# Kernel tuning notes

Measured on AMD Instinct MI355X. Metric: run time of the kernel, lower is better.

## Reference

```python
import jax, jax.numpy as jnp
import numpy as np

B, S, H, D = 2, 2048, 16, 64


def setup_inputs() -> dict:
    key = jax.random.key(0)
    ks = jax.random.split(key, 6)
    query = jax.random.normal(ks[0], (B, S, H, D), dtype=jnp.float32)
    k = jax.random.normal(ks[1], (B, S, H, D), dtype=jnp.float32)
    v = jax.random.normal(ks[2], (B, S, H, D), dtype=jnp.float32)
    r = jax.random.normal(ks[3], (B, S, H, D), dtype=jnp.float32)
    r_bias = jax.random.normal(ks[4], (H, D), dtype=jnp.float32)
    r_w_bias = jax.random.normal(ks[5], (H, D), dtype=jnp.float32)
    # causal mask, broadcast over batch and heads; mask==0 positions are filled with -1e9
    mask = jnp.tril(jnp.ones((S, S), dtype=jnp.int32))[None, None, :, :]
    return {"query": query, "key": k, "value": v, "r": r,
            "r_bias": r_bias, "r_w_bias": r_w_bias, "mask": mask}


def reference(query, key, value, r, r_bias, r_w_bias, mask):
    b, s, h, d = query.shape
    # content-based and position-based query terms (Transformer-XL u/v biases)
    rw_head_q = jnp.transpose(query + r_w_bias, (0, 2, 1, 3))  # [B,H,S,D]
    rr_head_q = jnp.transpose(query + r_bias, (0, 2, 1, 3))    # [B,H,S,D]
    k_t = jnp.transpose(key, (0, 2, 1, 3))                     # [B,H,S,D]
    r_t = jnp.transpose(r.reshape(b, -1, h, d), (0, 2, 1, 3))  # [B,H,R,D]
    AC = jnp.einsum('bhqd,bhkd->bhqk', rw_head_q, k_t)
    BD = jnp.einsum('bhqd,bhkd->bhqk', rr_head_q, r_t)
    scores = (AC + BD) * (1.0 / np.sqrt(d).astype(np.float32))
    scores = jnp.where(mask == 0, jnp.float32(-1e9), scores)
    p_attn = jax.nn.softmax(scores, axis=-1)
    v_t = jnp.transpose(value, (0, 2, 1, 3))                   # [B,H,S,D]
    out = jnp.einsum('bhqk,bhkd->bhqd', p_attn, v_t)
    return out, p_attn
```

## Files before the change

kernel.cpp:

```cpp
#include <hip/hip_runtime.h>
#include <hip/hip_fp16.h>

#define S_LEN 2048
#define DHEAD 64
#define NBH   32
#define NHEADS 16

typedef _Float16 half_t;
typedef half_t half8  __attribute__((ext_vector_type(8)));
typedef half_t half4v __attribute__((ext_vector_type(4)));
typedef __fp16 fp16x2 __attribute__((ext_vector_type(2)));
typedef float  f32x16 __attribute__((ext_vector_type(16)));
typedef float  f32x4  __attribute__((ext_vector_type(4)));

#define QSCALE 0.18033688011112042f

__global__ __launch_bounds__(256) void prep_kernel(
    const float* __restrict__ q, const float* __restrict__ k,
    const float* __restrict__ v, const float* __restrict__ r,
    const float* __restrict__ r_bias, const float* __restrict__ r_w_bias,
    half_t* __restrict__ qh, half_t* __restrict__ krh,
    half_t* __restrict__ vt, float* __restrict__ c2)
{
    __shared__ float vtile[64][65];
    int blk = blockIdx.x;
    int st  = blk & 31;
    int bh  = blk >> 5;
    int b = bh >> 4, h = bh & 15;
    int s0 = st * 64;
    int t = threadIdx.x;
    int dg = t & 15;
    int rw = t >> 4;
    const float4 ub = *(const float4*)(r_w_bias + h * 64 + 4 * dg);
    const float4 vb = *(const float4*)(r_bias   + h * 64 + 4 * dg);
    #pragma unroll
    for (int ps = 0; ps < 4; ++ps) {
        int row = ps * 16 + rw;
        size_t iidx = ((size_t)((b * S_LEN + s0 + row) * NHEADS + h)) * DHEAD + 4 * dg;
        float4 qv = *(const float4*)(q + iidx);
        float4 kv = *(const float4*)(k + iidx);
        float4 rv = *(const float4*)(r + iidx);
        float4 vv = *(const float4*)(v + iidx);
        size_t oidx = ((size_t)(bh * S_LEN + s0 + row)) * DHEAD + 4 * dg;
        half4v hq  = { (half_t)(qv.x * QSCALE), (half_t)(qv.y * QSCALE),
                       (half_t)(qv.z * QSCALE), (half_t)(qv.w * QSCALE) };
        half4v hkr = { (half_t)(kv.x + rv.x), (half_t)(kv.y + rv.y),
                       (half_t)(kv.z + rv.z), (half_t)(kv.w + rv.w) };
        *(half4v*)(qh  + oidx) = hq;
        *(half4v*)(krh + oidx) = hkr;
        vtile[4 * dg + 0][row] = vv.x;
        vtile[4 * dg + 1][row] = vv.y;
        vtile[4 * dg + 2][row] = vv.z;
        vtile[4 * dg + 3][row] = vv.w;
        float part = ub.x * kv.x + ub.y * kv.y + ub.z * kv.z + ub.w * kv.w
                   + vb.x * rv.x + vb.y * rv.y + vb.z * rv.z + vb.w * rv.w;
        #pragma unroll
        for (int mm = 1; mm <= 8; mm <<= 1) part += __shfl_xor(part, mm, 64);
        if (dg == 0) c2[(size_t)bh * S_LEN + s0 + row] = part * QSCALE;
    }
    __syncthreads();
    {
        int d = t >> 2, j0 = (t & 3) * 16;
        const float* src = &vtile[d][j0];
        half8 h0, h1;
        #pragma unroll
        for (int e = 0; e < 8; ++e) { h0[e] = (half_t)src[e]; h1[e] = (half_t)src[8 + e]; }
        half_t* dst = vt + ((size_t)(bh * DHEAD + d)) * S_LEN + s0 + j0;
        *(half8*)(dst)     = h0;
        *(half8*)(dst + 8) = h1;
    }
}

__global__ __launch_bounds__(256) void attn_kernel(
    const half_t* __restrict__ qh, const half_t* __restrict__ krh,
    const half_t* __restrict__ vt, const float* __restrict__ c2,
    float* __restrict__ dout)
{
    __shared__ float zl[4][64];
    __shared__ f32x4 pvred[2][8][64];

    int bb  = blockIdx.x;
    int bh  = (bb & 7) * 4 + ((bb >> 3) & 3);
    int qt  = 63 - (bb >> 5);
    int i0  = qt * 32;
    int w    = threadIdx.x >> 6;
    int lane = threadIdx.x & 63;
    int lo = lane & 31, hi = lane >> 5;
    int qrow = i0 + lo;

    const half_t* qp = qh  + ((size_t)(bh * S_LEN + i0)) * DHEAD;
    const half_t* kp = krh + ((size_t)bh * S_LEN) * DHEAD;
    const half_t* vp = vt  + ((size_t)bh * DHEAD) * S_LEN;
    const float*  cp = c2  + (size_t)bh * S_LEN;
    float* pout = dout + (size_t)NBH * S_LEN * DHEAD
                       + (size_t)bh * S_LEN * S_LEN
                       + (size_t)qrow * S_LEN + 4 * hi;
    float* oout = dout + ((size_t)(bh * S_LEN + i0)) * DHEAD;

    {
        f32x4 zz = {};
        for (int tt = qt + 1 + w; tt < 64; tt += 4) {
            #pragma unroll
            for (int g = 0; g < 4; ++g)
                *(f32x4*)(pout + tt * 32 + 8 * g) = zz;
        }
    }

    half8 qf[4];
    #pragma unroll
    for (int ds = 0; ds < 4; ++ds)
        qf[ds] = *(const half8*)(qp + lo * DHEAD + ds * 16 + hi * 8);

    auto loadK = [&](half8* kf, int t) {
        const half_t* base = kp + (size_t)(t * 32 + lo) * DHEAD + hi * 8;
        #pragma unroll
        for (int ds = 0; ds < 4; ++ds)
            kf[ds] = *(const half8*)(base + ds * 16);
    };
    auto loadV = [&](half8* vv, int t) {
        const half_t* r0 = vp + (size_t)lo * S_LEN + t * 32 + hi * 8;
        const half_t* r1 = vp + (size_t)(lo + 32) * S_LEN + t * 32 + hi * 8;
        vv[0] = *(const half8*)(r0);
        vv[1] = *(const half8*)(r0 + 16);
        vv[2] = *(const half8*)(r1);
        vv[3] = *(const half8*)(r1 + 16);
    };
    auto scoreT = [&](const half8* kf) {
        f32x16 acc = {};
        #pragma unroll
        for (int ds = 0; ds < 4; ++ds)
            acc = __builtin_amdgcn_mfma_f32_32x32x16_f16(kf[ds], qf[ds], acc, 0, 0, 0);
        return acc;
    };

    float Zs = 0.f;
    auto zTile = [&](int t, const half8* kf) {
        f32x16 acc = scoreT(kf);
        int jb = t * 32;
        float zs = 0.f;
        #pragma unroll
        for (int g = 0; g < 4; ++g) {
            f32x4 cv = *(const f32x4*)(cp + jb + 8 * g + 4 * hi);
            #pragma unroll
            for (int e = 0; e < 4; ++e) {
                float ev = exp2f(acc[4 * g + e] + cv[e]);
                if (t == qt) {
                    int j = jb + e + 8 * g + 4 * hi;
                    if (j > qrow) ev = 0.f;
                }
                zs += ev;
            }
        }
        Zs += zs;
    };
    {
        half8 kfA[4], kfB[4];
        int t = w;
        if (t <= qt) loadK(kfA, t);
        while (t <= qt) {
            if (t + 4 <= qt) loadK(kfB, t + 4);
            zTile(t, kfA);
            t += 4;
            if (t > qt) break;
            if (t + 4 <= qt) loadK(kfA, t + 4);
            zTile(t, kfB);
            t += 4;
        }
    }
    zl[w][lane] = Zs;
    __syncthreads();
    float Zrow = 0.f;
    #pragma unroll
    for (int w2 = 0; w2 < 4; ++w2) Zrow += zl[w2][lo] + zl[w2][lo + 32];
    float L = log2f(Zrow);

    f32x16 oa0 = {}, oa1 = {};
    auto pvTile = [&](int t, const half8* kf, const half8* vv) {
        f32x16 acc = scoreT(kf);
        int jb = t * 32;
        float p[16];
        #pragma unroll
        for (int g = 0; g < 4; ++g) {
            f32x4 cv = *(const f32x4*)(cp + jb + 8 * g + 4 * hi);
            #pragma unroll
            for (int e = 0; e < 4; ++e)
                p[4 * g + e] = exp2f(acc[4 * g + e] + cv[e] - L);
        }
        if (t == qt) {
            #pragma unroll
            for (int xx = 0; xx < 16; ++xx) {
                int j = jb + (xx & 3) + 8 * (xx >> 2) + 4 * hi;
                if (j > qrow) p[xx] = 0.f;
            }
        }
        #pragma unroll
        for (int g = 0; g < 4; ++g) {
            f32x4 st4 = { p[4 * g], p[4 * g + 1], p[4 * g + 2], p[4 * g + 3] };
            *(f32x4*)(pout + jb + 8 * g) = st4;
        }
        unsigned int wds[8];
        #pragma unroll
        for (int g2 = 0; g2 < 8; ++g2) {
            union { fp16x2 h; unsigned int u; } pk;
            pk.h = __builtin_amdgcn_cvt_pkrtz(p[2 * g2], p[2 * g2 + 1]);
            wds[g2] = pk.u;
        }
        unsigned int pw[8];
        #pragma unroll
        for (int g2 = 0; g2 < 8; ++g2) pw[g2] = __shfl_xor(wds[g2], 32, 64);
        union { unsigned int uu[4]; half8 h; } pa0, pa1;
        pa0.uu[0] = hi ? pw[2]  : wds[0];
        pa0.uu[1] = hi ? pw[3]  : wds[1];
        pa0.uu[2] = hi ? wds[2] : pw[0];
        pa0.uu[3] = hi ? wds[3] : pw[1];
        pa1.uu[0] = hi ? pw[6]  : wds[4];
        pa1.uu[1] = hi ? pw[7]  : wds[5];
        pa1.uu[2] = hi ? wds[6] : pw[4];
        pa1.uu[3] = hi ? wds[7] : pw[5];
        oa0 = __builtin_amdgcn_mfma_f32_32x32x16_f16(pa0.h, vv[0], oa0, 0, 0, 0);
        oa0 = __builtin_amdgcn_mfma_f32_32x32x16_f16(pa1.h, vv[1], oa0, 0, 0, 0);
        oa1 = __builtin_amdgcn_mfma_f32_32x32x16_f16(pa0.h, vv[2], oa1, 0, 0, 0);
        oa1 = __builtin_amdgcn_mfma_f32_32x32x16_f16(pa1.h, vv[3], oa1, 0, 0, 0);
    };
    {
        half8 kfA[4], kfB[4], vA[4], vB[4];
        int t = w;
        if (t <= qt) { loadK(kfA, t); loadV(vA, t); }
        while (t <= qt) {
            if (t + 4 <= qt) { loadK(kfB, t + 4); loadV(vB, t + 4); }
            pvTile(t, kfA, vA);
            t += 4;
            if (t > qt) break;
            if (t + 4 <= qt) { loadK(kfA, t + 4); loadV(vA, t + 4); }
            pvTile(t, kfB, vB);
            t += 4;
        }
    }

    __syncthreads();
    if (w >= 2) {
        #pragma unroll
        for (int j = 0; j < 4; ++j) {
            f32x4 c0 = { oa0[4*j], oa0[4*j+1], oa0[4*j+2], oa0[4*j+3] };
            f32x4 c1 = { oa1[4*j], oa1[4*j+1], oa1[4*j+2], oa1[4*j+3] };
            pvred[w - 2][j][lane]     = c0;
            pvred[w - 2][j + 4][lane] = c1;
        }
    }
    __syncthreads();
    if (w < 2) {
        #pragma unroll
        for (int j = 0; j < 4; ++j) {
            f32x4 c0 = pvred[w][j][lane];
            f32x4 c1 = pvred[w][j + 4][lane];
            #pragma unroll
            for (int e = 0; e < 4; ++e) { oa0[4*j+e] += c0[e]; oa1[4*j+e] += c1[e]; }
        }
    }
    __syncthreads();
    if (w == 1) {
        #pragma unroll
        for (int j = 0; j < 4; ++j) {
            f32x4 c0 = { oa0[4*j], oa0[4*j+1], oa0[4*j+2], oa0[4*j+3] };
            f32x4 c1 = { oa1[4*j], oa1[4*j+1], oa1[4*j+2], oa1[4*j+3] };
            pvred[0][j][lane]     = c0;
            pvred[0][j + 4][lane] = c1;
        }
    }
    __syncthreads();
    if (w == 0) {
        #pragma unroll
        for (int j = 0; j < 4; ++j) {
            f32x4 c0 = pvred[0][j][lane];
            f32x4 c1 = pvred[0][j + 4][lane];
            #pragma unroll
            for (int e = 0; e < 4; ++e) { oa0[4*j+e] += c0[e]; oa1[4*j+e] += c1[e]; }
        }
        #pragma unroll
        for (int xx = 0; xx < 16; ++xx) {
            int row = (xx & 3) + 8 * (xx >> 2) + 4 * hi;
            oout[(size_t)row * DHEAD + lo]      = oa0[xx];
            oout[(size_t)row * DHEAD + 32 + lo] = oa1[xx];
        }
    }
}

extern "C" void kernel_launch(void* const* d_in, const int* in_sizes, int n_in,
                              void* d_out, int out_size, void* d_ws, size_t ws_size,
                              hipStream_t stream)
{
    const float* q   = (const float*)d_in[0];
    const float* k   = (const float*)d_in[1];
    const float* v   = (const float*)d_in[2];
    const float* r   = (const float*)d_in[3];
    const float* rb  = (const float*)d_in[4];
    const float* rwb = (const float*)d_in[5];
    float* out = (float*)d_out;

    char* ws = (char*)d_ws;
    half_t* qh  = (half_t*)(ws);
    half_t* krh = (half_t*)(ws + (size_t) 8 * 1024 * 1024);
    half_t* vtp = (half_t*)(ws + (size_t)16 * 1024 * 1024);
    float*  c2  = (float*) (ws + (size_t)24 * 1024 * 1024);

    hipLaunchKernelGGL(prep_kernel, dim3(1024), dim3(256), 0, stream,
                       q, k, v, r, rb, rwb, qh, krh, vtp, c2);
    hipLaunchKernelGGL(attn_kernel, dim3(2048), dim3(256), 0, stream,
                       qh, krh, vtp, c2, out);
}
```

Measured before the change: 706.9 us.

## Split attention into separate normalizer and probability/PV kernels

The fused attention kernel becomes two launches. The first computes each row's log-sum-exp normalizer and zero-fills the masked upper part of P. The second recomputes the scores, writes P and accumulates P·V using the stored normalizer. The bias term (and the subtracted normalizer) now seeds the MFMA accumulator instead of being added after it. The explicit double-buffered K/V prefetch is replaced by simple per-iteration loads. The aim is lower register pressure and higher occupancy in each kernel, at the cost of an extra launch, a workspace round trip for the normalizer, and losing the manual load/compute overlap.

New measurement: 743.2 us. 1.05x slower.

```diff
diff --git a/kernel.cpp b/kernel.cpp
--- a/kernel.cpp
+++ b/kernel.cpp
@@ -71,14 +71,12 @@
     }
 }
 
-__global__ __launch_bounds__(256) void attn_kernel(
+__global__ __launch_bounds__(256) void zpass_kernel(
     const half_t* __restrict__ qh, const half_t* __restrict__ krh,
-    const half_t* __restrict__ vt, const float* __restrict__ c2,
+    const float* __restrict__ c2, float* __restrict__ Lws,
     float* __restrict__ dout)
 {
     __shared__ float zl[4][64];
-    __shared__ f32x4 pvred[2][8][64];
-
     int bb  = blockIdx.x;
     int bh  = (bb & 7) * 4 + ((bb >> 3) & 3);
     int qt  = 63 - (bb >> 5);
@@ -90,6 +88,81 @@
 
     const half_t* qp = qh  + ((size_t)(bh * S_LEN + i0)) * DHEAD;
     const half_t* kp = krh + ((size_t)bh * S_LEN) * DHEAD;
+    const float*  cp = c2  + (size_t)bh * S_LEN;
+    float* pout = dout + (size_t)NBH * S_LEN * DHEAD
+                       + (size_t)bh * S_LEN * S_LEN
+                       + (size_t)qrow * S_LEN + 4 * hi;
+
+    {
+        f32x4 zz = {};
+        for (int tt = qt + 1 + w; tt < 64; tt += 4) {
+            #pragma unroll
+            for (int g = 0; g < 4; ++g)
+                *(f32x4*)(pout + tt * 32 + 8 * g) = zz;
+        }
+    }
+
+    half8 qf[4];
+    #pragma unroll
+    for (int ds = 0; ds < 4; ++ds)
+        qf[ds] = *(const half8*)(qp + lo * DHEAD + ds * 16 + hi * 8);
+
+    float Zs = 0.f;
+    for (int t = w; t <= qt; t += 4) {
+        const half_t* base = kp + (size_t)(t * 32 + lo) * DHEAD + hi * 8;
+        half8 kf[4];
+        #pragma unroll
+        for (int ds = 0; ds < 4; ++ds) kf[ds] = *(const half8*)(base + ds * 16);
+        int jb = t * 32;
+        f32x16 acc;
+        #pragma unroll
+        for (int g = 0; g < 4; ++g) {
+            f32x4 cv = *(const f32x4*)(cp + jb + 8 * g + 4 * hi);
+            #pragma unroll
+            for (int e = 0; e < 4; ++e) acc[4 * g + e] = cv[e];
+        }
+        #pragma unroll
+        for (int ds = 0; ds < 4; ++ds)
+            acc = __builtin_amdgcn_mfma_f32_32x32x16_f16(kf[ds], qf[ds], acc, 0, 0, 0);
+        float zs = 0.f;
+        #pragma unroll
+        for (int xx = 0; xx < 16; ++xx) {
+            float ev = exp2f(acc[xx]);
+            if (t == qt) {
+                int j = jb + (xx & 3) + 8 * (xx >> 2) + 4 * hi;
+                if (j > qrow) ev = 0.f;
+            }
+            zs += ev;
+        }
+        Zs += zs;
+    }
+    zl[w][lane] = Zs;
+    __syncthreads();
+    if (w == 0) {
+        float Zrow = 0.f;
+        #pragma unroll
+        for (int w2 = 0; w2 < 4; ++w2) Zrow += zl[w2][lo] + zl[w2][lo + 32];
+        if (hi == 0) Lws[(size_t)bh * S_LEN + qrow] = log2f(Zrow);
+    }
+}
+
+__global__ __launch_bounds__(256) void ppass_kernel(
+    const half_t* __restrict__ qh, const half_t* __restrict__ krh,
+    const half_t* __restrict__ vt, const float* __restrict__ c2,
+    const float* __restrict__ Lws, float* __restrict__ dout)
+{
+    __shared__ f32x4 pvred[2][8][64];
+    int bb  = blockIdx.x;
+    int bh  = (bb & 7) * 4 + ((bb >> 3) & 3);
+    int qt  = 63 - (bb >> 5);
+    int i0  = qt * 32;
+    int w    = threadIdx.x >> 6;
+    int lane = threadIdx.x & 63;
+    int lo = lane & 31, hi = lane >> 5;
+    int qrow = i0 + lo;
+
+    const half_t* qp = qh  + ((size_t)(bh * S_LEN + i0)) * DHEAD;
+    const half_t* kp = krh + ((size_t)bh * S_LEN) * DHEAD;
     const half_t* vp = vt  + ((size_t)bh * DHEAD) * S_LEN;
     const float*  cp = c2  + (size_t)bh * S_LEN;
     float* pout = dout + (size_t)NBH * S_LEN * DHEAD
@@ -97,95 +170,41 @@
                        + (size_t)qrow * S_LEN + 4 * hi;
     float* oout = dout + ((size_t)(bh * S_LEN + i0)) * DHEAD;
 
-    {
-        f32x4 zz = {};
-        for (int tt = qt + 1 + w; tt < 64; tt += 4) {
-            #pragma unroll
-            for (int g = 0; g < 4; ++g)
-                *(f32x4*)(pout + tt * 32 + 8 * g) = zz;
-        }
-    }
+    float Lq = Lws[(size_t)bh * S_LEN + qrow];
 
     half8 qf[4];
     #pragma unroll
     for (int ds = 0; ds < 4; ++ds)
         qf[ds] = *(const half8*)(qp + lo * DHEAD + ds * 16 + hi * 8);
 
-    auto loadK = [&](half8* kf, int t) {
-        const half_t* base = kp + (size_t)(t * 32 + lo) * DHEAD + hi * 8;
-        #pragma unroll
-        for (int ds = 0; ds < 4; ++ds)
-            kf[ds] = *(const half8*)(base + ds * 16);
-    };
-    auto loadV = [&](half8* vv, int t) {
+    f32x16 oa0 = {}, oa1 = {};
+    for (int t = w; t <= qt; t += 4) {
+        const half_t* kbase = kp + (size_t)(t * 32 + lo) * DHEAD + hi * 8;
+        half8 kf[4];
+        #pragma unroll
+        for (int ds = 0; ds < 4; ++ds) kf[ds] = *(const half8*)(kbase + ds * 16);
         const half_t* r0 = vp + (size_t)lo * S_LEN + t * 32 + hi * 8;
         const half_t* r1 = vp + (size_t)(lo + 32) * S_LEN + t * 32 + hi * 8;
-        vv[0] = *(const half8*)(r0);
-        vv[1] = *(const half8*)(r0 + 16);
-        vv[2] = *(const half8*)(r1);
-        vv[3] = *(const half8*)(r1 + 16);
-    };
-    auto scoreT = [&](const half8* kf) {
-        f32x16 acc = {};
+        half8 v0 = *(const half8*)(r0);
+        half8 v1 = *(const half8*)(r0 + 16);
+        half8 v2 = *(const half8*)(r1);
+        half8 v3 = *(const half8*)(r1 + 16);
+
+        int jb = t * 32;
+        f32x16 acc;
+        #pragma unroll
+        for (int g = 0; g < 4; ++g) {
+            f32x4 cv = *(const f32x4*)(cp + jb + 8 * g + 4 * hi);
+            #pragma unroll
+            for (int e = 0; e < 4; ++e) acc[4 * g + e] = cv[e] - Lq;
+        }
         #pragma unroll
         for (int ds = 0; ds < 4; ++ds)
             acc = __builtin_amdgcn_mfma_f32_32x32x16_f16(kf[ds], qf[ds], acc, 0, 0, 0);
-        return acc;
-    };
-
-    float Zs = 0.f;
-    auto zTile = [&](int t, const half8* kf) {
-        f32x16 acc = scoreT(kf);
-        int jb = t * 32;
-        float zs = 0.f;
-        #pragma unroll
-        for (int g = 0; g < 4; ++g) {
-            f32x4 cv = *(const f32x4*)(cp + jb + 8 * g + 4 * hi);
-            #pragma unroll
-            for (int e = 0; e < 4; ++e) {
-                float ev = exp2f(acc[4 * g + e] + cv[e]);
-                if (t == qt) {
-                    int j = jb + e + 8 * g + 4 * hi;
-                    if (j > qrow) ev = 0.f;
-                }
-                zs += ev;
-            }
-        }
-        Zs += zs;
-    };
-    {
-        half8 kfA[4], kfB[4];
-        int t = w;
-        if (t <= qt) loadK(kfA, t);
-        while (t <= qt) {
-            if (t + 4 <= qt) loadK(kfB, t + 4);
-            zTile(t, kfA);
-            t += 4;
-            if (t > qt) break;
-            if (t + 4 <= qt) loadK(kfA, t + 4);
-            zTile(t, kfB);
-            t += 4;
-        }
-    }
-    zl[w][lane] = Zs;
-    __syncthreads();
-    float Zrow = 0.f;
-    #pragma unroll
-    for (int w2 = 0; w2 < 4; ++w2) Zrow += zl[w2][lo] + zl[w2][lo + 32];
-    float L = log2f(Zrow);
-
-    f32x16 oa0 = {}, oa1 = {};
-    auto pvTile = [&](int t, const half8* kf, const half8* vv) {
-        f32x16 acc = scoreT(kf);
-        int jb = t * 32;
+
         float p[16];
         #pragma unroll
-        for (int g = 0; g < 4; ++g) {
-            f32x4 cv = *(const f32x4*)(cp + jb + 8 * g + 4 * hi);
-            #pragma unroll
-            for (int e = 0; e < 4; ++e)
-                p[4 * g + e] = exp2f(acc[4 * g + e] + cv[e] - L);
-        }
+        for (int xx = 0; xx < 16; ++xx) p[xx] = exp2f(acc[xx]);
         if (t == qt) {
             #pragma unroll
             for (int xx = 0; xx < 16; ++xx) {
@@ -217,27 +236,12 @@
         pa1.uu[1] = hi ? pw[7]  : wds[5];
         pa1.uu[2] = hi ? wds[6] : pw[4];
         pa1.uu[3] = hi ? wds[7] : pw[5];
-        oa0 = __builtin_amdgcn_mfma_f32_32x32x16_f16(pa0.h, vv[0], oa0, 0, 0, 0);
-        oa0 = __builtin_amdgcn_mfma_f32_32x32x16_f16(pa1.h, vv[1], oa0, 0, 0, 0);
-        oa1 = __builtin_amdgcn_mfma_f32_32x32x16_f16(pa0.h, vv[2], oa1, 0, 0, 0);
-        oa1 = __builtin_amdgcn_mfma_f32_32x32x16_f16(pa1.h, vv[3], oa1, 0, 0, 0);
-    };
-    {
-        half8 kfA[4], kfB[4], vA[4], vB[4];
-        int t = w;
-        if (t <= qt) { loadK(kfA, t); loadV(vA, t); }
-        while (t <= qt) {
-            if (t + 4 <= qt) { loadK(kfB, t + 4); loadV(vB, t + 4); }
-            pvTile(t, kfA, vA);
-            t += 4;
-            if (t > qt) break;
-            if (t + 4 <= qt) { loadK(kfA, t + 4); loadV(vA, t + 4); }
-            pvTile(t, kfB, vB);
-            t += 4;
-        }
-    }
-
-    __syncthreads();
+        oa0 = __builtin_amdgcn_mfma_f32_32x32x16_f16(pa0.h, v0, oa0, 0, 0, 0);
+        oa0 = __builtin_amdgcn_mfma_f32_32x32x16_f16(pa1.h, v1, oa0, 0, 0, 0);
+        oa1 = __builtin_amdgcn_mfma_f32_32x32x16_f16(pa0.h, v2, oa1, 0, 0, 0);
+        oa1 = __builtin_amdgcn_mfma_f32_32x32x16_f16(pa1.h, v3, oa1, 0, 0, 0);
+    }
+
     if (w >= 2) {
         #pragma unroll
         for (int j = 0; j < 4; ++j) {
@@ -302,9 +306,12 @@
     half_t* krh = (half_t*)(ws + (size_t) 8 * 1024 * 1024);
     half_t* vtp = (half_t*)(ws + (size_t)16 * 1024 * 1024);
     float*  c2  = (float*) (ws + (size_t)24 * 1024 * 1024);
+    float*  Lws = (float*) (ws + (size_t)24 * 1024 * 1024 + 256 * 1024);
 
     hipLaunchKernelGGL(prep_kernel, dim3(1024), dim3(256), 0, stream,
                        q, k, v, r, rb, rwb, qh, krh, vtp, c2);
-    hipLaunchKernelGGL(attn_kernel, dim3(2048), dim3(256), 0, stream,
-                       qh, krh, vtp, c2, out);
+    hipLaunchKernelGGL(zpass_kernel, dim3(2048), dim3(256), 0, stream,
+                       qh, krh, c2, Lws, out);
+    hipLaunchKernelGGL(ppass_kernel, dim3(2048), dim3(256), 0, stream,
+                       qh, krh, vtp, c2, Lws, out);
 }
```
